# Optimization experiments

Hardware: AMD Instinct MI355X
Metric: run time of the kernel (lower is better)

The kernel has to match this reference:

```python
import jax, jax.numpy as jnp
import numpy as np
from jax import lax

THR = 1.0
SLOPE = 25.0
EPS = 1e-5

@jax.custom_vjp
def spike(u):
    # Heaviside with fast-sigmoid surrogate gradient (slope=25)
    return (u > 0.0).astype(u.dtype)

def _spike_fwd(u):
    return (u > 0.0).astype(u.dtype), u

def _spike_bwd(u, g):
    return (g / (SLOPE * jnp.abs(u) + 1.0) ** 2,)

spike.defvjp(_spike_fwd, _spike_bwd)

def lif_scan(inp, beta):
    # inp: (T, B, H); snntorch Leaky, reset_mechanism='subtract', init mem=0
    def step(mem, cur):
        reset = lax.stop_gradient(spike(mem - THR))
        mem = beta * mem + cur - reset * THR
        spk = spike(mem - THR)
        return mem, (spk, mem)
    mem0 = jnp.zeros(inp.shape[1:], inp.dtype)
    _, (spk, mem) = lax.scan(step, mem0, inp)
    return spk, mem

def bn_per_step(h, g, b):
    # h: (T, B, H); training-mode BatchNorm1d applied per timestep over batch
    m = h.mean(axis=1, keepdims=True)
    v = h.var(axis=1, keepdims=True)
    return (h - m) / jnp.sqrt(v + EPS) * g + b

def setup_inputs() -> dict:
    key = jax.random.key(0)
    ks = jax.random.split(key, 16)
    B, T, C = 128, 128, 32
    H, Ts, HOR, K = 512, 4, 96, 3
    s = 0.02
    return {
        "x": jax.random.normal(ks[0], (B, T, C), jnp.float32),
        "conv_w": jax.random.normal(ks[1], (H * Ts, C, K), jnp.float32) * s,
        "conv_b": jnp.zeros((H * Ts,), jnp.float32),
        "bn1_g": jnp.ones((H * Ts,), jnp.float32),
        "bn1_b": jnp.zeros((H * Ts,), jnp.float32),
        "beta_enc": jnp.full((H,), 0.9, jnp.float32),
        "bn2_g": jnp.ones((H,), jnp.float32),
        "bn2_b": jnp.zeros((H,), jnp.float32),
        "beta2": jnp.full((H,), 0.9, jnp.float32),
        "bn3_g": jnp.ones((H,), jnp.float32),
        "bn3_b": jnp.zeros((H,), jnp.float32),
        "beta3": jnp.full((H,), 0.9, jnp.float32),
        "wq": jax.random.normal(ks[2], (H, H), jnp.float32) * s,
        "bq": jnp.zeros((H,), jnp.float32),
        "wk": jax.random.normal(ks[3], (H, H), jnp.float32) * s,
        "bk": jnp.zeros((H,), jnp.float32),
        "wv": jax.random.normal(ks[4], (H, H), jnp.float32) * s,
        "bv": jnp.zeros((H,), jnp.float32),
        "bna_g": jnp.ones((H,), jnp.float32),
        "bna_b": jnp.zeros((H,), jnp.float32),
        "wh": jax.random.normal(ks[5], (HOR, H), jnp.float32) * s,
        "bh": jnp.zeros((HOR,), jnp.float32),
    }

def reference(x, conv_w, conv_b, bn1_g, bn1_b, beta_enc, bn2_g, bn2_b, beta2,
              bn3_g, bn3_b, beta3, wq, bq, wk, bk, wv, bv, bna_g, bna_b, wh, bh):
    B, T, C = x.shape
    H = beta2.shape[0]
    Ts = conv_w.shape[0] // H
    # Conv spike encoder: Conv1d(C -> H*Ts, k, pad=k//2)
    k = conv_w.shape[2]
    h = lax.conv_general_dilated(x.transpose(0, 2, 1), conv_w, (1,), [(k // 2, k // 2)],
                                 dimension_numbers=("NCH", "OIH", "NCH"))
    h = h + conv_b[None, :, None]  # (B, H*Ts, T)
    # BatchNorm1d (training mode): stats over (B, T) per channel, biased var
    m = h.mean((0, 2), keepdims=True)
    v = h.var((0, 2), keepdims=True)
    h = (h - m) / jnp.sqrt(v + EPS) * bn1_g[None, :, None] + bn1_b[None, :, None]
    # (B, H*Ts, T) -> (T*Ts, B, H)
    h = h.transpose(0, 2, 1).reshape(B, T, Ts, H).reshape(B, T * Ts, H).transpose(1, 0, 2)
    spk_enc, _ = lif_scan(h, jnp.clip(beta_enc, 0.0, 0.99))
    # bn2 -> lif2 -> bn3 -> lif3 (BN applied per step in the torch loop)
    h2 = bn_per_step(spk_enc, bn2_g, bn2_b)
    s2, _ = lif_scan(h2, jnp.clip(beta2, 0.0, 0.99))
    h3 = bn_per_step(s2, bn3_g, bn3_b)
    _, mem3 = lif_scan(h3, jnp.clip(beta3, 0.0, 0.99))  # (Ttot, B, H)
    # Spiking attention over membrane trajectory
    xa = mem3.transpose(1, 0, 2)  # (B, Ttot, H)
    Q = xa @ wq.T + bq
    K = xa @ wk.T + bk
    V = xa @ wv.T + bv
    attn = jax.nn.sigmoid(jnp.einsum("btd,bsd->bts", Q, K) * (H ** -0.5))
    feat = jnp.einsum("bts,bsd->btd", attn, V).mean(axis=1)  # (B, H)
    mf = feat.mean(0, keepdims=True)
    vf = feat.var(0, keepdims=True)
    feat = (feat - mf) / jnp.sqrt(vf + EPS) * bna_g + bna_b
    return feat @ wh.T + bh  # (B, horizon)
```

## Files before the change

kernel.cpp:

```cpp
#include <hip/hip_runtime.h>
#include <math.h>

#define EPSF 1e-5f

static constexpr int Bn   = 128;
static constexpr int Tn   = 128;
static constexpr int Cn   = 32;
static constexpr int On   = 2048;
static constexpr int Hn   = 512;
static constexpr int TTn  = 512;
static constexpr int HORn = 96;
static constexpr int BH   = Bn * Hn;
static constexpr float THRf = 1.0f;

__device__ __forceinline__ float bf2f(unsigned short u) {
    union { unsigned int i; float f; } v; v.i = ((unsigned int)u) << 16; return v.f;
}
__device__ __forceinline__ unsigned short f2bf(float f) {
    union { float f; unsigned int i; } v; v.f = f;
    unsigned int r = v.i + 0x7fff + ((v.i >> 16) & 1);
    return (unsigned short)(r >> 16);
}

using bfrag  = __attribute__((ext_vector_type(8))) short;
using f32x4v = __attribute__((ext_vector_type(4))) float;
using us8v   = __attribute__((ext_vector_type(8))) unsigned short;

#define GLD16(gp, lp) __builtin_amdgcn_global_load_lds( \
    (const __attribute__((address_space(1))) void*)(gp), \
    (__attribute__((address_space(3))) void*)(lp), 16, 0, 0)

__global__ __launch_bounds__(256) void im2col_k(const float* __restrict__ x,
    unsigned short* __restrict__ Ph, unsigned short* __restrict__ Pl)
{
    int idx = blockIdx.x * 256 + threadIdx.x;
    int row = idx / 96, kc = idx - row * 96;
    int k = kc >> 5, c = kc & 31;
    int t = row & 127, b = row >> 7;
    int tg = t + k - 1;
    float v = (tg >= 0 && tg < Tn) ? x[((size_t)b * Tn + tg) * Cn + c] : 0.f;
    unsigned short hi = f2bf(v);
    Ph[idx] = hi;
    Pl[idx] = f2bf(v - bf2f(hi));
}

__global__ __launch_bounds__(256) void wprep_k(const float* __restrict__ wconv,
    unsigned short* __restrict__ Wh, unsigned short* __restrict__ Wl)
{
    int idx = blockIdx.x * 256 + threadIdx.x;
    int o = idx / 96, kc = idx - o * 96;
    int k = kc >> 5, c = kc & 31;
    float v = wconv[(size_t)o * 96 + c * 3 + k];
    unsigned short hi = f2bf(v);
    Wh[idx] = hi;
    Wl[idx] = f2bf(v - bf2f(hi));
}

__global__ __launch_bounds__(256) void conv_mfma_k(
    const unsigned short* __restrict__ Ph, const unsigned short* __restrict__ Pl,
    const unsigned short* __restrict__ Wh, const unsigned short* __restrict__ Wl,
    float* __restrict__ raw, float* __restrict__ sums)
{
    const int b  = blockIdx.x;
    const int n0 = blockIdx.y * 128;
    const int tid = threadIdx.x;
    const int lane = tid & 63;
    const int quad = lane >> 4, lr = lane & 15;
    const int wid = tid >> 6, wm = wid & 1, wn = wid >> 1;

    f32x4v acc[4][4] = {};
#pragma unroll
    for (int ks = 0; ks < 3; ks++) {
        const int col = ks * 32 + quad * 8;
        bfrag ah[4], al[4], bh[4], bl[4];
#pragma unroll
        for (int mi = 0; mi < 4; mi++) {
            size_t roff = ((size_t)b * 128 + wm * 64 + mi * 16 + lr) * 96 + col;
            ah[mi] = *(const bfrag*)(Ph + roff);
            al[mi] = *(const bfrag*)(Pl + roff);
        }
#pragma unroll
        for (int ni = 0; ni < 4; ni++) {
            size_t roff = (size_t)(n0 + wn * 64 + ni * 16 + lr) * 96 + col;
            bh[ni] = *(const bfrag*)(Wh + roff);
            bl[ni] = *(const bfrag*)(Wl + roff);
        }
#pragma unroll
        for (int mi = 0; mi < 4; mi++)
#pragma unroll
            for (int ni = 0; ni < 4; ni++) {
                acc[mi][ni] = __builtin_amdgcn_mfma_f32_16x16x32_bf16(
                    ah[mi], bh[ni], acc[mi][ni], 0, 0, 0);
                acc[mi][ni] = __builtin_amdgcn_mfma_f32_16x16x32_bf16(
                    ah[mi], bl[ni], acc[mi][ni], 0, 0, 0);
                acc[mi][ni] = __builtin_amdgcn_mfma_f32_16x16x32_bf16(
                    al[mi], bh[ni], acc[mi][ni], 0, 0, 0);
            }
    }
#pragma unroll
    for (int ni = 0; ni < 4; ni++) {
        int o = n0 + wn * 64 + ni * 16 + lr;
        int ts = o >> 9, hh = o & 511;
        float s = 0.f, ss = 0.f;
#pragma unroll
        for (int mi = 0; mi < 4; mi++)
#pragma unroll
            for (int r = 0; r < 4; r++) {
                int t = wm * 64 + mi * 16 + quad * 4 + r;
                float v = acc[mi][ni][r];
                raw[((size_t)(t * 4 + ts) * Bn + b) * Hn + hh] = v;
                s += v; ss += v * v;
            }
        s  += __shfl_xor(s, 16);  s  += __shfl_xor(s, 32);
        ss += __shfl_xor(ss, 16); ss += __shfl_xor(ss, 32);
        if (quad == 0) {
            atomicAdd(&sums[o], s);
            atomicAdd(&sums[On + o], ss);
        }
    }
}

__global__ void bn1_final_k(const float* __restrict__ sums,
                            const float* __restrict__ g, const float* __restrict__ bb,
                            float* __restrict__ scale, float* __restrict__ shift)
{
    int o = blockIdx.x * 256 + threadIdx.x;
    float m = sums[o] * (1.f / 16384.f);
    float v = sums[On + o] * (1.f / 16384.f) - m * m;
    float sc = g[o] / sqrtf(v + EPSF);
    scale[o] = sc;
    shift[o] = bb[o] - m * sc;
}

__global__ __launch_bounds__(256) void lif1_k(const float* __restrict__ raw,
    const float* __restrict__ scale, const float* __restrict__ shift,
    const float* __restrict__ beta_in, unsigned char* __restrict__ spk)
{
    const int thr = blockIdx.x * 256 + threadIdx.x;
    const int hh = thr & 511;
    const float beta = fminf(fmaxf(beta_in[hh], 0.f), 0.99f);
    float sc[4], sh[4];
#pragma unroll
    for (int ts = 0; ts < 4; ts++) { sc[ts] = scale[ts * Hn + hh]; sh[ts] = shift[ts * Hn + hh]; }
    float mem = 0.f;
    for (int tt = 0; tt < TTn; tt += 8) {
        float cu[8];
#pragma unroll
        for (int u = 0; u < 8; u++) cu[u] = raw[(size_t)(tt + u) * BH + thr];
#pragma unroll
        for (int u = 0; u < 8; u++) {
            float cur = cu[u] * sc[u & 3] + sh[u & 3];
            float reset = mem > THRf ? 1.f : 0.f;
            mem = beta * mem + cur - reset;
            spk[(size_t)(tt + u) * BH + thr] = mem > THRf ? (unsigned char)1 : (unsigned char)0;
        }
    }
}

__global__ __launch_bounds__(256) void bnstep_k(const unsigned char* __restrict__ spk,
    const float* __restrict__ g, const float* __restrict__ bb,
    float* __restrict__ av, float* __restrict__ zv)
{
    const int tt = blockIdx.x;
    const int h0 = threadIdx.x * 2;
    int c0 = 0, c1 = 0;
    const unsigned char* base = spk + (size_t)tt * BH + h0;
#pragma unroll 8
    for (int b = 0; b < Bn; b++) {
        unsigned short v = *(const unsigned short*)(base + (size_t)b * Hn);
        c0 += (v & 0xff); c1 += (v >> 8);
    }
#pragma unroll
    for (int q = 0; q < 2; q++) {
        int hh = h0 + q;
        float p = (q ? c1 : c0) * (1.f / 128.f);
        float inv = 1.f / sqrtf(p - p * p + EPSF);
        float gi = g[hh] * inv;
        float zz = bb[hh] - p * gi;
        av[(size_t)tt * Hn + hh] = gi + zz;
        zv[(size_t)tt * Hn + hh] = zz;
    }
}

__global__ __launch_bounds__(256) void lif2_k(const unsigned char* __restrict__ sin_,
    const float* __restrict__ av, const float* __restrict__ zv,
    const float* __restrict__ beta_in, unsigned char* __restrict__ sout)
{
    const int thr = blockIdx.x * 256 + threadIdx.x;
    const int hh = thr & 511;
    const float beta = fminf(fmaxf(beta_in[hh], 0.f), 0.99f);
    float mem = 0.f;
    for (int tt = 0; tt < TTn; tt += 8) {
        float aa[8], zz[8]; unsigned char ss[8];
#pragma unroll
        for (int u = 0; u < 8; u++) {
            ss[u] = sin_[(size_t)(tt + u) * BH + thr];
            aa[u] = av[(size_t)(tt + u) * Hn + hh];
            zz[u] = zv[(size_t)(tt + u) * Hn + hh];
        }
#pragma unroll
        for (int u = 0; u < 8; u++) {
            float cur = ss[u] ? aa[u] : zz[u];
            float reset = mem > THRf ? 1.f : 0.f;
            mem = beta * mem + cur - reset;
            sout[(size_t)(tt + u) * BH + thr] = mem > THRf ? (unsigned char)1 : (unsigned char)0;
        }
    }
}

__global__ __launch_bounds__(256) void lif3_k(const unsigned char* __restrict__ sin_,
    const float* __restrict__ av, const float* __restrict__ zv,
    const float* __restrict__ beta_in, unsigned short* __restrict__ mem3b)
{
    const int thr = blockIdx.x * 256 + threadIdx.x;
    const int hh = thr & 511;
    const int b = thr >> 9;
    const float beta = fminf(fmaxf(beta_in[hh], 0.f), 0.99f);
    float mem = 0.f;
    for (int tt = 0; tt < TTn; tt += 8) {
        float aa[8], zz[8]; unsigned char ss[8];
#pragma unroll
        for (int u = 0; u < 8; u++) {
            ss[u] = sin_[(size_t)(tt + u) * BH + thr];
            aa[u] = av[(size_t)(tt + u) * Hn + hh];
            zz[u] = zv[(size_t)(tt + u) * Hn + hh];
        }
#pragma unroll
        for (int u = 0; u < 8; u++) {
            float cur = ss[u] ? aa[u] : zz[u];
            float reset = mem > THRf ? 1.f : 0.f;
            mem = beta * mem + cur - reset;
            mem3b[((size_t)b * TTn + (tt + u)) * Hn + hh] = f2bf(mem);
        }
    }
}

__global__ __launch_bounds__(256) void gemm_atb_k(const float* __restrict__ Aw,
    const float* __restrict__ Bw, float* __restrict__ GTp)
{
    __shared__ float As[8][132];
    __shared__ float Bs[8][132];
    const int m0 = blockIdx.x * 128;
    const int n0 = blockIdx.y * 128;
    const int kz = blockIdx.z;
    const int tid = threadIdx.x;
    const int ir = tid >> 5, cl = (tid & 31) * 4;
    const float* Ap = Aw + (size_t)ir * 512 + m0 + cl;
    const float* Bp = Bw + (size_t)ir * 512 + n0 + cl;
    const int tm = tid & 15, tn = tid >> 4;
    float acc[8][8];
#pragma unroll
    for (int i = 0; i < 8; i++)
#pragma unroll
        for (int j = 0; j < 8; j++) acc[i][j] = 0.f;

    for (int i0 = kz * 64; i0 < kz * 64 + 64; i0 += 8) {
        const float4 avv = *(const float4*)(Ap + (size_t)i0 * 512);
        const float4 bvv = *(const float4*)(Bp + (size_t)i0 * 512);
        __syncthreads();
        *(float4*)&As[ir][cl] = avv;
        *(float4*)&Bs[ir][cl] = bvv;
        __syncthreads();
#pragma unroll
        for (int kk = 0; kk < 8; kk++) {
            float4 a0 = *(const float4*)&As[kk][tm * 8];
            float4 a1 = *(const float4*)&As[kk][tm * 8 + 4];
            float4 b0 = *(const float4*)&Bs[kk][tn * 8];
            float4 b1 = *(const float4*)&Bs[kk][tn * 8 + 4];
            float a_[8] = {a0.x, a0.y, a0.z, a0.w, a1.x, a1.y, a1.z, a1.w};
            float b_[8] = {b0.x, b0.y, b0.z, b0.w, b1.x, b1.y, b1.z, b1.w};
#pragma unroll
            for (int i = 0; i < 8; i++)
#pragma unroll
                for (int j = 0; j < 8; j++) acc[i][j] += a_[i] * b_[j];
        }
    }
    float* outp = GTp + (size_t)kz * Hn * Hn;
#pragma unroll
    for (int i = 0; i < 8; i++) {
        size_t rowoff = (size_t)(m0 + tm * 8 + i) * 512 + n0 + tn * 8;
#pragma unroll
        for (int j = 0; j < 8; j++) outp[rowoff + j] = acc[i][j];
    }
}

__global__ void gtred_k(const float* __restrict__ GTp, unsigned short* __restrict__ GT)
{
    int idx = blockIdx.x * 256 + threadIdx.x;
    float s = 0.f;
#pragma unroll
    for (int z = 0; z < 8; z++) s += GTp[(size_t)z * Hn * Hn + idx];
    GT[idx] = f2bf(s);
}

__global__ __launch_bounds__(256) void bias_prep_k(const float* __restrict__ wq,
    const float* __restrict__ wk, const float* __restrict__ bq,
    const float* __restrict__ bk, float* __restrict__ qb, float* __restrict__ kb)
{
    const int blk = blockIdx.x;
    const bool doq = blk < 8;
    const int d0 = (doq ? blk : blk - 8) * 64;
    const float* W    = doq ? wq : wk;
    const float* bvec = doq ? bk : bq;
    const int dl = threadIdx.x & 63, ig = threadIdx.x >> 6;
    float s = 0.f;
    for (int i = ig * 128; i < ig * 128 + 128; i++)
        s += W[(size_t)i * 512 + d0 + dl] * bvec[i];
    __shared__ float red[4][64];
    red[ig][dl] = s;
    __syncthreads();
    if (ig == 0)
        (doq ? qb : kb)[d0 + dl] = red[0][dl] + red[1][dl] + red[2][dl] + red[3][dl];
}

__global__ void c0_k(const float* __restrict__ bq, const float* __restrict__ bk,
                     float* __restrict__ c0)
{
    __shared__ float red[256];
    float p = 0.f;
    for (int i = threadIdx.x; i < 512; i += 256) p += bq[i] * bk[i];
    red[threadIdx.x] = p;
    __syncthreads();
    for (int s = 128; s > 0; s >>= 1) {
        if (threadIdx.x < s) red[threadIdx.x] += red[threadIdx.x + s];
        __syncthreads();
    }
    if (threadIdx.x == 0) c0[0] = red[0];
}

__global__ __launch_bounds__(256) void ygemm_k(const unsigned short* __restrict__ A,
    const unsigned short* __restrict__ Bsrc, const float* __restrict__ qb,
    const float* __restrict__ kb, const float* __restrict__ c0,
    unsigned short* __restrict__ C, float* __restrict__ rowq,
    float* __restrict__ rowk)
{
    __shared__ unsigned short As[128 * 32];
    __shared__ unsigned short Bs[128 * 32];
    const int m0 = blockIdx.x * 128;
    const int n0 = blockIdx.y * 128;
    const int tid = threadIdx.x;
    const int lane = tid & 63;
    const int quad = lane >> 4, lr = lane & 15;
    const int wid = tid >> 6;
    const int wm = wid & 1, wn = wid >> 1;

    const int srow   = wid * 32 + (lane >> 2);
    const int schunk = (lane & 3) ^ ((lane >> 3) & 3);
    const unsigned short* gA0 = A    + (size_t)(m0 + srow) * 512 + schunk * 8;
    const unsigned short* gA1 = gA0 + (size_t)16 * 512;
    const unsigned short* gB0 = Bsrc + (size_t)(n0 + srow) * 512 + schunk * 8;
    const unsigned short* gB1 = gB0 + (size_t)16 * 512;
    unsigned short* lA0 = As + wid * 32 * 32;
    unsigned short* lA1 = lA0 + 16 * 32;
    unsigned short* lB0 = Bs + wid * 32 * 32;
    unsigned short* lB1 = lB0 + 16 * 32;

    const int rslot = quad ^ ((lr >> 1) & 3);
    const bool dorows = (blockIdx.y == 0) && (wn == 0);
    float rq_acc[4] = {0.f, 0.f, 0.f, 0.f};
    float rk_acc[4] = {0.f, 0.f, 0.f, 0.f};

    f32x4v acc[4][4] = {};
    for (int k0 = 0; k0 < 512; k0 += 32) {
        __syncthreads();
        GLD16(gA0 + k0, lA0);
        GLD16(gA1 + k0, lA1);
        GLD16(gB0 + k0, lB0);
        GLD16(gB1 + k0, lB1);
        __syncthreads();
        bfrag af[4], bf_[4];
#pragma unroll
        for (int mi = 0; mi < 4; mi++)
            af[mi] = *(const bfrag*)&As[(wm * 64 + mi * 16 + lr) * 32 + rslot * 8];
#pragma unroll
        for (int ni = 0; ni < 4; ni++)
            bf_[ni] = *(const bfrag*)&Bs[(wn * 64 + ni * 16 + lr) * 32 + rslot * 8];
#pragma unroll
        for (int mi = 0; mi < 4; mi++)
#pragma unroll
            for (int ni = 0; ni < 4; ni++)
                acc[mi][ni] = __builtin_amdgcn_mfma_f32_16x16x32_bf16(
                    af[mi], bf_[ni], acc[mi][ni], 0, 0, 0);
        if (dorows) {
            const float4 qv0 = *(const float4*)(qb + k0 + quad * 8);
            const float4 qv1 = *(const float4*)(qb + k0 + quad * 8 + 4);
            const float4 kv0 = *(const float4*)(kb + k0 + quad * 8);
            const float4 kv1 = *(const float4*)(kb + k0 + quad * 8 + 4);
            const float qv[8] = {qv0.x, qv0.y, qv0.z, qv0.w, qv1.x, qv1.y, qv1.z, qv1.w};
            const float kv[8] = {kv0.x, kv0.y, kv0.z, kv0.w, kv1.x, kv1.y, kv1.z, kv1.w};
#pragma unroll
            for (int mi = 0; mi < 4; mi++)
#pragma unroll
                for (int j = 0; j < 8; j++) {
                    float a = bf2f((unsigned short)af[mi][j]);
                    rq_acc[mi] += a * qv[j];
                    rk_acc[mi] += a * kv[j];
                }
        }
    }
#pragma unroll
    for (int mi = 0; mi < 4; mi++)
#pragma unroll
        for (int ni = 0; ni < 4; ni++) {
            int col = n0 + wn * 64 + ni * 16 + lr;
#pragma unroll
            for (int r = 0; r < 4; r++) {
                int row = m0 + wm * 64 + mi * 16 + quad * 4 + r;
                C[(size_t)row * 512 + col] = f2bf(acc[mi][ni][r]);
            }
        }
    if (dorows) {
        const float c0v = c0[0];
#pragma unroll
        for (int mi = 0; mi < 4; mi++) {
            float rq = rq_acc[mi], rk = rk_acc[mi];
            rq += __shfl_xor(rq, 16); rq += __shfl_xor(rq, 32);
            rk += __shfl_xor(rk, 16); rk += __shfl_xor(rk, 32);
            if (quad == 0) {
                int row = m0 + wm * 64 + mi * 16 + lr;
                rowq[row] = rq + c0v;
                rowk[row] = rk;
            }
        }
    }
}

__global__ __launch_bounds__(256) void scores_k(const unsigned short* __restrict__ Y,
    const unsigned short* __restrict__ Xm, const float* __restrict__ rowq,
    const float* __restrict__ rowk, float* __restrict__ wacc)
{
    __shared__ unsigned short As[128 * 32];
    __shared__ unsigned short Bs[128 * 32];
    __shared__ float colsum[128];
    __shared__ float rq_s[128], rk_s[128];
    const int b  = blockIdx.z;
    const int m0 = blockIdx.x * 128;
    const int n0 = blockIdx.y * 128;
    const int tid = threadIdx.x;
    const int lane = tid & 63;
    const int quad = lane >> 4, lr = lane & 15;
    const int wid = tid >> 6;
    const int wm = wid & 1, wn = wid >> 1;

    if (tid < 128) {
        colsum[tid] = 0.f;
        rq_s[tid] = rowq[(size_t)b * TTn + m0 + tid];
        rk_s[tid] = rowk[(size_t)b * TTn + n0 + tid];
    }

    const int srow   = wid * 32 + (lane >> 2);
    const int schunk = (lane & 3) ^ ((lane >> 3) & 3);
    const unsigned short* gA0 = Y  + (size_t)b * TTn * Hn + (size_t)(m0 + srow) * 512 + schunk * 8;
    const unsigned short* gA1 = gA0 + (size_t)16 * 512;
    const unsigned short* gB0 = Xm + (size_t)b * TTn * Hn + (size_t)(n0 + srow) * 512 + schunk * 8;
    const unsigned short* gB1 = gB0 + (size_t)16 * 512;
    unsigned short* lA0 = As + wid * 32 * 32;
    unsigned short* lA1 = lA0 + 16 * 32;
    unsigned short* lB0 = Bs + wid * 32 * 32;
    unsigned short* lB1 = lB0 + 16 * 32;
    const int rslot = quad ^ ((lr >> 1) & 3);

    f32x4v acc[4][4] = {};
    for (int k0 = 0; k0 < 512; k0 += 32) {
        __syncthreads();
        GLD16(gA0 + k0, lA0);
        GLD16(gA1 + k0, lA1);
        GLD16(gB0 + k0, lB0);
        GLD16(gB1 + k0, lB1);
        __syncthreads();
        bfrag af[4], bf_[4];
#pragma unroll
        for (int mi = 0; mi < 4; mi++)
            af[mi] = *(const bfrag*)&As[(wm * 64 + mi * 16 + lr) * 32 + rslot * 8];
#pragma unroll
        for (int ni = 0; ni < 4; ni++)
            bf_[ni] = *(const bfrag*)&Bs[(wn * 64 + ni * 16 + lr) * 32 + rslot * 8];
#pragma unroll
        for (int mi = 0; mi < 4; mi++)
#pragma unroll
            for (int ni = 0; ni < 4; ni++)
                acc[mi][ni] = __builtin_amdgcn_mfma_f32_16x16x32_bf16(
                    af[mi], bf_[ni], acc[mi][ni], 0, 0, 0);
    }
    const float scl = 0.044194173824159216f;
#pragma unroll
    for (int ni = 0; ni < 4; ni++) {
        float s_ln = 0.f;
        float rkv = rk_s[wn * 64 + ni * 16 + lr];
#pragma unroll
        for (int mi = 0; mi < 4; mi++) {
#pragma unroll
            for (int r = 0; r < 4; r++) {
                float rqv = rq_s[wm * 64 + mi * 16 + quad * 4 + r];
                float xv = (acc[mi][ni][r] + rqv + rkv) * scl;
                s_ln += 1.f / (1.f + __expf(-xv));
            }
        }
        atomicAdd(&colsum[wn * 64 + ni * 16 + lr], s_ln);
    }
    __syncthreads();
    if (tid < 128)
        atomicAdd(&wacc[(size_t)b * TTn + n0 + tid], colsum[tid] * (1.f / 512.f));
}

__global__ __launch_bounds__(256) void wsum_k(const float* __restrict__ wacc,
    const unsigned short* __restrict__ mem3b, float* __restrict__ u,
    float* __restrict__ W1)
{
    const int b = blockIdx.x;
    const int tid = threadIdx.x;
    __shared__ float ws_[512];
    __shared__ float red[256];
    ws_[tid] = wacc[(size_t)b * TTn + tid];
    ws_[tid + 256] = wacc[(size_t)b * TTn + tid + 256];
    __syncthreads();
    red[tid] = ws_[tid] + ws_[tid + 256];
    __syncthreads();
    for (int s = 128; s > 0; s >>= 1) {
        if (tid < s) red[tid] += red[tid + s];
        __syncthreads();
    }
    if (tid == 0) W1[b] = red[0];
    float a0 = 0.f, a1 = 0.f;
    const unsigned short* Xb = mem3b + (size_t)b * TTn * Hn;
    for (int s = 0; s < TTn; s++) {
        float w = ws_[s];
        a0 += w * bf2f(Xb[(size_t)s * Hn + tid]);
        a1 += w * bf2f(Xb[(size_t)s * Hn + tid + 256]);
    }
    u[(size_t)b * Hn + tid] = a0;
    u[(size_t)b * Hn + tid + 256] = a1;
}

__global__ __launch_bounds__(256) void feat2_k(const float* __restrict__ u,
    const float* __restrict__ W1, const float* __restrict__ wv,
    const float* __restrict__ bv, float* __restrict__ feat)
{
    const int b = blockIdx.x;
    const int tid = threadIdx.x;
    __shared__ float us[512];
    us[tid] = u[(size_t)b * Hn + tid];
    us[tid + 256] = u[(size_t)b * Hn + tid + 256];
    __syncthreads();
    const float w1 = W1[b];
#pragma unroll
    for (int q = 0; q < 2; q++) {
        int d = tid + q * 256;
        float acc = bv[d] * w1;
        const float* wr = wv + (size_t)d * 512;
        for (int e = 0; e < 512; e += 4) {
            float4 w4 = *(const float4*)(wr + e);
            acc += us[e] * w4.x + us[e+1] * w4.y + us[e+2] * w4.z + us[e+3] * w4.w;
        }
        feat[(size_t)b * Hn + d] = acc;
    }
}

__global__ void bna_k(const float* __restrict__ feat, const float* __restrict__ g,
                      const float* __restrict__ bb, float* __restrict__ featn)
{
    int d = blockIdx.x * 256 + threadIdx.x;
    float s = 0.f, ss = 0.f;
    for (int b = 0; b < Bn; b++) { float v = feat[(size_t)b * Hn + d]; s += v; ss += v * v; }
    float m = s * (1.f / 128.f);
    float var = ss * (1.f / 128.f) - m * m;
    float sc = g[d] / sqrtf(var + EPSF);
    float sh = bb[d] - m * sc;
    for (int b = 0; b < Bn; b++) featn[(size_t)b * Hn + d] = feat[(size_t)b * Hn + d] * sc + sh;
}

__global__ __launch_bounds__(128) void head_k(const float* __restrict__ featn,
    const float* __restrict__ wh, const float* __restrict__ bh, float* __restrict__ out)
{
    const int b = blockIdx.x;
    __shared__ float f[512];
    const int tid = threadIdx.x;
    for (int i = tid; i < 512; i += 128) f[i] = featn[(size_t)b * Hn + i];
    __syncthreads();
    if (tid < HORn) {
        float accv = bh[tid];
        const float* wr = wh + (size_t)tid * Hn;
        for (int d = 0; d < 512; d++) accv += f[d] * wr[d];
        out[(size_t)b * HORn + tid] = accv;
    }
}

__global__ void dbg_k(float* out, float v) { out[0] = v; }

extern "C" void kernel_launch(void* const* d_in, const int* in_sizes, int n_in,
                              void* d_out, int out_size, void* d_ws, size_t ws_size,
                              hipStream_t stream)
{
    (void)in_sizes; (void)n_in;
    const float* x      = (const float*)d_in[0];
    const float* conv_w = (const float*)d_in[1];
    const float* bn1_g  = (const float*)d_in[3];
    const float* bn1_b  = (const float*)d_in[4];
    const float* beta_e = (const float*)d_in[5];
    const float* bn2_g  = (const float*)d_in[6];
    const float* bn2_b  = (const float*)d_in[7];
    const float* beta2  = (const float*)d_in[8];
    const float* bn3_g  = (const float*)d_in[9];
    const float* bn3_b  = (const float*)d_in[10];
    const float* beta3  = (const float*)d_in[11];
    const float* wq     = (const float*)d_in[12];
    const float* bq     = (const float*)d_in[13];
    const float* wk     = (const float*)d_in[14];
    const float* bk     = (const float*)d_in[15];
    const float* wv     = (const float*)d_in[16];
    const float* bv     = (const float*)d_in[17];
    const float* bna_g  = (const float*)d_in[18];
    const float* bna_b  = (const float*)d_in[19];
    const float* wh     = (const float*)d_in[20];
    const float* bh     = (const float*)d_in[21];
    float* out = (float*)d_out;

    char* ws = (char*)d_ws;
    size_t off = 0;
    auto alloc = [&](size_t bytes) {
        char* p = ws + off;
        off += (bytes + 255) & ~(size_t)255;
        return p;
    };
    float* raw          = (float*)alloc((size_t)TTn * BH * 4);
    unsigned char* spk1 = (unsigned char*)alloc((size_t)TTn * BH);
    unsigned char* s2   = (unsigned char*)alloc((size_t)TTn * BH);
    unsigned short* Ph = (unsigned short*)alloc((size_t)Bn * Tn * 96 * 2);
    unsigned short* Pl = (unsigned short*)alloc((size_t)Bn * Tn * 96 * 2);
    unsigned short* Wh = (unsigned short*)alloc((size_t)On * 96 * 2);
    unsigned short* Wl = (unsigned short*)alloc((size_t)On * 96 * 2);
    float* sums   = (float*)alloc(2 * On * 4);
    float* scale1 = (float*)alloc(On * 4);
    float* shift1 = (float*)alloc(On * 4);
    float* a2     = (float*)alloc((size_t)TTn * Hn * 4);
    float* z2     = (float*)alloc((size_t)TTn * Hn * 4);
    float* a3     = (float*)alloc((size_t)TTn * Hn * 4);
    float* z3     = (float*)alloc((size_t)TTn * Hn * 4);
    float* wacc   = (float*)alloc((size_t)Bn * TTn * 4);
    float* GTp    = (float*)alloc((size_t)8 * Hn * Hn * 4);
    unsigned short* GT = (unsigned short*)alloc((size_t)Hn * Hn * 2);
    float* qb     = (float*)alloc(Hn * 4);
    float* kb     = (float*)alloc(Hn * 4);
    float* c0     = (float*)alloc(256);
    float* rowq   = (float*)alloc((size_t)Bn * TTn * 4);
    float* rowk   = (float*)alloc((size_t)Bn * TTn * 4);
    float* u      = (float*)alloc((size_t)Bn * Hn * 4);
    float* W1     = (float*)alloc(Bn * 4);
    float* feat   = (float*)alloc((size_t)Bn * Hn * 4);
    float* featn  = (float*)alloc((size_t)Bn * Hn * 4);
    unsigned short* mem3b = (unsigned short*)raw;
    unsigned short* Y     = (unsigned short*)spk1;

    if (ws_size < off) {
        hipMemsetAsync(d_out, 0, (size_t)out_size * 4, stream);
        dbg_k<<<1, 1, 0, stream>>>(out, (float)ws_size);
        return;
    }

    hipMemsetAsync(sums, 0, 2 * On * 4, stream);
    hipMemsetAsync(wacc, 0, (size_t)Bn * TTn * 4, stream);

    im2col_k<<<(Bn * Tn * 96) / 256, 256, 0, stream>>>(x, Ph, Pl);
    wprep_k<<<(On * 96) / 256, 256, 0, stream>>>(conv_w, Wh, Wl);
    conv_mfma_k<<<dim3(Bn, On / 128), 256, 0, stream>>>(Ph, Pl, Wh, Wl, raw, sums);
    bn1_final_k<<<On / 256, 256, 0, stream>>>(sums, bn1_g, bn1_b, scale1, shift1);
    lif1_k<<<BH / 256, 256, 0, stream>>>(raw, scale1, shift1, beta_e, spk1);
    bnstep_k<<<TTn, 256, 0, stream>>>(spk1, bn2_g, bn2_b, a2, z2);
    lif2_k<<<BH / 256, 256, 0, stream>>>(spk1, a2, z2, beta2, s2);
    bnstep_k<<<TTn, 256, 0, stream>>>(s2, bn3_g, bn3_b, a3, z3);
    lif3_k<<<BH / 256, 256, 0, stream>>>(s2, a3, z3, beta3, mem3b);
    gemm_atb_k<<<dim3(4, 4, 8), 256, 0, stream>>>(wk, wq, GTp);
    gtred_k<<<(Hn * Hn) / 256, 256, 0, stream>>>(GTp, GT);
    bias_prep_k<<<16, 256, 0, stream>>>(wq, wk, bq, bk, qb, kb);
    c0_k<<<1, 256, 0, stream>>>(bq, bk, c0);
    ygemm_k<<<dim3((Bn * TTn) / 128, Hn / 128), 256, 0, stream>>>(
        mem3b, GT, qb, kb, c0, Y, rowq, rowk);
    scores_k<<<dim3(TTn / 128, TTn / 128, Bn), 256, 0, stream>>>(Y, mem3b, rowq, rowk, wacc);
    wsum_k<<<Bn, 256, 0, stream>>>(wacc, mem3b, u, W1);
    feat2_k<<<Bn, 256, 0, stream>>>(u, W1, wv, bv, feat);
    bna_k<<<Hn / 256, 256, 0, stream>>>(feat, bna_g, bna_b, featn);
    head_k<<<Bn, 128, 0, stream>>>(featn, wh, bh, out);
}
```

Before: 540.3 us.

## Restructure Y GEMM to keep full A rows in LDS and widen scores K-step

The Y GEMM now loads a full 64x512 row block of A into shared memory once per block. It streams GT fragments straight from global memory with register double-buffering, and each block covers all 512 output columns. This removes the per-K-step barriers and the repeated A reloads across column tiles. The scores kernel doubles its K tile to 64, which halves the number of barrier pairs but doubles its LDS footprint. The 64KB LDS in ygemm and the uncached global B loads may reduce occupancy.

```diff
diff --git a/kernel.cpp b/kernel.cpp
--- a/kernel.cpp
+++ b/kernel.cpp
@@ -329,86 +329,93 @@
 }
 
 __global__ __launch_bounds__(256) void ygemm_k(const unsigned short* __restrict__ A,
-    const unsigned short* __restrict__ Bsrc, const float* __restrict__ qb,
+    const unsigned short* __restrict__ GT, const float* __restrict__ qb,
     const float* __restrict__ kb, const float* __restrict__ c0,
     unsigned short* __restrict__ C, float* __restrict__ rowq,
     float* __restrict__ rowk)
 {
-    __shared__ unsigned short As[128 * 32];
-    __shared__ unsigned short Bs[128 * 32];
-    const int m0 = blockIdx.x * 128;
-    const int n0 = blockIdx.y * 128;
+    __shared__ unsigned short Afull[64 * 512];
+    const int m0 = blockIdx.x * 64;
     const int tid = threadIdx.x;
     const int lane = tid & 63;
     const int quad = lane >> 4, lr = lane & 15;
     const int wid = tid >> 6;
-    const int wm = wid & 1, wn = wid >> 1;
-
-    const int srow   = wid * 32 + (lane >> 2);
-    const int schunk = (lane & 3) ^ ((lane >> 3) & 3);
-    const unsigned short* gA0 = A    + (size_t)(m0 + srow) * 512 + schunk * 8;
-    const unsigned short* gA1 = gA0 + (size_t)16 * 512;
-    const unsigned short* gB0 = Bsrc + (size_t)(n0 + srow) * 512 + schunk * 8;
-    const unsigned short* gB1 = gB0 + (size_t)16 * 512;
-    unsigned short* lA0 = As + wid * 32 * 32;
-    unsigned short* lA1 = lA0 + 16 * 32;
-    unsigned short* lB0 = Bs + wid * 32 * 32;
-    unsigned short* lB1 = lB0 + 16 * 32;
-
-    const int rslot = quad ^ ((lr >> 1) & 3);
-    const bool dorows = (blockIdx.y == 0) && (wn == 0);
+
+#pragma unroll
+    for (int i = 0; i < 16; i++) {
+        const int r = wid * 16 + i;
+        const int cc = lane ^ (i & 7);
+        GLD16(A + (size_t)(m0 + r) * 512 + cc * 8, Afull + r * 512);
+    }
+    __syncthreads();
+
+    const bool dorows = (wid == 0);
     float rq_acc[4] = {0.f, 0.f, 0.f, 0.f};
     float rk_acc[4] = {0.f, 0.f, 0.f, 0.f};
 
-    f32x4v acc[4][4] = {};
-    for (int k0 = 0; k0 < 512; k0 += 32) {
-        __syncthreads();
-        GLD16(gA0 + k0, lA0);
-        GLD16(gA1 + k0, lA1);
-        GLD16(gB0 + k0, lB0);
-        GLD16(gB1 + k0, lB1);
-        __syncthreads();
-        bfrag af[4], bf_[4];
+#pragma unroll
+    for (int n0t = 0; n0t < 2; n0t++) {
+        const int nbase = n0t * 256 + wid * 64;
+        const unsigned short* pb[4];
+#pragma unroll
+        for (int ni = 0; ni < 4; ni++)
+            pb[ni] = GT + (size_t)(nbase + ni * 16 + lr) * 512 + quad * 8;
+        f32x4v acc[4][4] = {};
+        bfrag bcur[4];
+#pragma unroll
+        for (int ni = 0; ni < 4; ni++) bcur[ni] = *(const bfrag*)pb[ni];
+#pragma unroll
+        for (int k0 = 0; k0 < 512; k0 += 32) {
+            bfrag bnxt[4];
+            if (k0 + 32 < 512) {
+#pragma unroll
+                for (int ni = 0; ni < 4; ni++)
+                    bnxt[ni] = *(const bfrag*)(pb[ni] + k0 + 32);
+            }
+            bfrag af[4];
+            const int slot = ((k0 >> 3) + quad) ^ (lr & 7);
+#pragma unroll
+            for (int mi = 0; mi < 4; mi++)
+                af[mi] = *(const bfrag*)&Afull[(mi * 16 + lr) * 512 + slot * 8];
+#pragma unroll
+            for (int mi = 0; mi < 4; mi++)
+#pragma unroll
+                for (int ni = 0; ni < 4; ni++)
+                    acc[mi][ni] = __builtin_amdgcn_mfma_f32_16x16x32_bf16(
+                        af[mi], bcur[ni], acc[mi][ni], 0, 0, 0);
+            if (dorows && n0t == 0) {
+                const float4 qv0 = *(const float4*)(qb + k0 + quad * 8);
+                const float4 qv1 = *(const float4*)(qb + k0 + quad * 8 + 4);
+                const float4 kv0 = *(const float4*)(kb + k0 + quad * 8);
+                const float4 kv1 = *(const float4*)(kb + k0 + quad * 8 + 4);
+                const float qv[8] = {qv0.x, qv0.y, qv0.z, qv0.w, qv1.x, qv1.y, qv1.z, qv1.w};
+                const float kv[8] = {kv0.x, kv0.y, kv0.z, kv0.w, kv1.x, kv1.y, kv1.z, kv1.w};
+#pragma unroll
+                for (int mi = 0; mi < 4; mi++)
+#pragma unroll
+                    for (int j = 0; j < 8; j++) {
+                        float a = bf2f((unsigned short)af[mi][j]);
+                        rq_acc[mi] += a * qv[j];
+                        rk_acc[mi] += a * kv[j];
+                    }
+            }
+            if (k0 + 32 < 512) {
+#pragma unroll
+                for (int ni = 0; ni < 4; ni++) bcur[ni] = bnxt[ni];
+            }
+        }
 #pragma unroll
         for (int mi = 0; mi < 4; mi++)
-            af[mi] = *(const bfrag*)&As[(wm * 64 + mi * 16 + lr) * 32 + rslot * 8];
-#pragma unroll
-        for (int ni = 0; ni < 4; ni++)
-            bf_[ni] = *(const bfrag*)&Bs[(wn * 64 + ni * 16 + lr) * 32 + rslot * 8];
-#pragma unroll
-        for (int mi = 0; mi < 4; mi++)
-#pragma unroll
-            for (int ni = 0; ni < 4; ni++)
-                acc[mi][ni] = __builtin_amdgcn_mfma_f32_16x16x32_bf16(
-                    af[mi], bf_[ni], acc[mi][ni], 0, 0, 0);
-        if (dorows) {
-            const float4 qv0 = *(const float4*)(qb + k0 + quad * 8);
-            const float4 qv1 = *(const float4*)(qb + k0 + quad * 8 + 4);
-            const float4 kv0 = *(const float4*)(kb + k0 + quad * 8);
-            const float4 kv1 = *(const float4*)(kb + k0 + quad * 8 + 4);
-            const float qv[8] = {qv0.x, qv0.y, qv0.z, qv0.w, qv1.x, qv1.y, qv1.z, qv1.w};
-            const float kv[8] = {kv0.x, kv0.y, kv0.z, kv0.w, kv1.x, kv1.y, kv1.z, kv1.w};
-#pragma unroll
-            for (int mi = 0; mi < 4; mi++)
-#pragma unroll
-                for (int j = 0; j < 8; j++) {
-                    float a = bf2f((unsigned short)af[mi][j]);
-                    rq_acc[mi] += a * qv[j];
-                    rk_acc[mi] += a * kv[j];
+#pragma unroll
+            for (int ni = 0; ni < 4; ni++) {
+                int col = nbase + ni * 16 + lr;
+#pragma unroll
+                for (int r = 0; r < 4; r++) {
+                    int row = m0 + mi * 16 + quad * 4 + r;
+                    C[(size_t)row * 512 + col] = f2bf(acc[mi][ni][r]);
                 }
-        }
-    }
-#pragma unroll
-    for (int mi = 0; mi < 4; mi++)
-#pragma unroll
-        for (int ni = 0; ni < 4; ni++) {
-            int col = n0 + wn * 64 + ni * 16 + lr;
-#pragma unroll
-            for (int r = 0; r < 4; r++) {
-                int row = m0 + wm * 64 + mi * 16 + quad * 4 + r;
-                C[(size_t)row * 512 + col] = f2bf(acc[mi][ni][r]);
-            }
-        }
+            }
+    }
     if (dorows) {
         const float c0v = c0[0];
 #pragma unroll
@@ -417,7 +424,7 @@
             rq += __shfl_xor(rq, 16); rq += __shfl_xor(rq, 32);
             rk += __shfl_xor(rk, 16); rk += __shfl_xor(rk, 32);
             if (quad == 0) {
-                int row = m0 + wm * 64 + mi * 16 + lr;
+                int row = m0 + mi * 16 + lr;
                 rowq[row] = rq + c0v;
                 rowk[row] = rk;
             }
@@ -429,8 +436,8 @@
     const unsigned short* __restrict__ Xm, const float* __restrict__ rowq,
     const float* __restrict__ rowk, float* __restrict__ wacc)
 {
-    __shared__ unsigned short As[128 * 32];
-    __shared__ unsigned short Bs[128 * 32];
+    __shared__ unsigned short As[128 * 64];
+    __shared__ unsigned short Bs[128 * 64];
     __shared__ float colsum[128];
     __shared__ float rq_s[128], rk_s[128];
     const int b  = blockIdx.z;
@@ -448,39 +455,39 @@
         rk_s[tid] = rowk[(size_t)b * TTn + n0 + tid];
     }
 
-    const int srow   = wid * 32 + (lane >> 2);
-    const int schunk = (lane & 3) ^ ((lane >> 3) & 3);
-    const unsigned short* gA0 = Y  + (size_t)b * TTn * Hn + (size_t)(m0 + srow) * 512 + schunk * 8;
-    const unsigned short* gA1 = gA0 + (size_t)16 * 512;
-    const unsigned short* gB0 = Xm + (size_t)b * TTn * Hn + (size_t)(n0 + srow) * 512 + schunk * 8;
-    const unsigned short* gB1 = gB0 + (size_t)16 * 512;
-    unsigned short* lA0 = As + wid * 32 * 32;
-    unsigned short* lA1 = lA0 + 16 * 32;
-    unsigned short* lB0 = Bs + wid * 32 * 32;
-    unsigned short* lB1 = lB0 + 16 * 32;
-    const int rslot = quad ^ ((lr >> 1) & 3);
+    const int srw = lane >> 3;
+    const int scc = (lane & 7) ^ (srw & 7);
+    const unsigned short* gA = Y  + (size_t)b * TTn * Hn
+        + (size_t)(m0 + wid * 32 + srw) * 512 + scc * 8;
+    const unsigned short* gB = Xm + (size_t)b * TTn * Hn
+        + (size_t)(n0 + wid * 32 + srw) * 512 + scc * 8;
 
     f32x4v acc[4][4] = {};
-    for (int k0 = 0; k0 < 512; k0 += 32) {
+    for (int k0 = 0; k0 < 512; k0 += 64) {
         __syncthreads();
-        GLD16(gA0 + k0, lA0);
-        GLD16(gA1 + k0, lA1);
-        GLD16(gB0 + k0, lB0);
-        GLD16(gB1 + k0, lB1);
+#pragma unroll
+        for (int j = 0; j < 4; j++) {
+            GLD16(gA + (size_t)j * 8 * 512 + k0, As + (wid * 32 + j * 8) * 64);
+            GLD16(gB + (size_t)j * 8 * 512 + k0, Bs + (wid * 32 + j * 8) * 64);
+        }
         __syncthreads();
-        bfrag af[4], bf_[4];
-#pragma unroll
-        for (int mi = 0; mi < 4; mi++)
-            af[mi] = *(const bfrag*)&As[(wm * 64 + mi * 16 + lr) * 32 + rslot * 8];
-#pragma unroll
-        for (int ni = 0; ni < 4; ni++)
-            bf_[ni] = *(const bfrag*)&Bs[(wn * 64 + ni * 16 + lr) * 32 + rslot * 8];
-#pragma unroll
-        for (int mi = 0; mi < 4; mi++)
+#pragma unroll
+        for (int kk = 0; kk < 2; kk++) {
+            const int slot = (kk * 4 + quad) ^ (lr & 7);
+            bfrag af[4], bf_[4];
+#pragma unroll
+            for (int mi = 0; mi < 4; mi++)
+                af[mi] = *(const bfrag*)&As[(wm * 64 + mi * 16 + lr) * 64 + slot * 8];
 #pragma unroll
             for (int ni = 0; ni < 4; ni++)
-                acc[mi][ni] = __builtin_amdgcn_mfma_f32_16x16x32_bf16(
-                    af[mi], bf_[ni], acc[mi][ni], 0, 0, 0);
+                bf_[ni] = *(const bfrag*)&Bs[(wn * 64 + ni * 16 + lr) * 64 + slot * 8];
+#pragma unroll
+            for (int mi = 0; mi < 4; mi++)
+#pragma unroll
+                for (int ni = 0; ni < 4; ni++)
+                    acc[mi][ni] = __builtin_amdgcn_mfma_f32_16x16x32_bf16(
+                        af[mi], bf_[ni], acc[mi][ni], 0, 0, 0);
+        }
     }
     const float scl = 0.044194173824159216f;
 #pragma unroll
@@ -673,7 +680,7 @@
     gtred_k<<<(Hn * Hn) / 256, 256, 0, stream>>>(GTp, GT);
     bias_prep_k<<<16, 256, 0, stream>>>(wq, wk, bq, bk, qb, kb);
     c0_k<<<1, 256, 0, stream>>>(bq, bk, c0);
-    ygemm_k<<<dim3((Bn * TTn) / 128, Hn / 128), 256, 0, stream>>>(
+    ygemm_k<<<(Bn * TTn) / 64, 256, 0, stream>>>(
         mem3b, GT, qb, kb, c0, Y, rowq, rowk);
     scores_k<<<dim3(TTn / 128, TTn / 128, Bn), 256, 0, stream>>>(Y, mem3b, rowq, rowk, wacc);
     wsum_k<<<Bn, 256, 0, stream>>>(wacc, mem3b, u, W1);
```

Result: no change. 550.1 us (+1.8%).
